# Kernel tuning notes

Measured on AMD Instinct MI355X. Metric: run time of the kernel, lower is better.

## Reference

```python
import jax, jax.numpy as jnp
import numpy as np

BATCH = 8
N_CLASSES = 3            # including background
PRE_NMS_LIMIT = 6000
NMS_THRESH = 0.5
SCALE = 512.0
WINDOW = (0.0, 0.0, 512.0, 512.0)   # y1, x1, y2, x2
STD_DEV = np.array([0.1, 0.1, 0.2, 0.2], np.float32)
GROUP_OFFSET = 4096.0    # > image extent; separates (batch, class) groups in NMS

_RATIOS = np.array([0.5, 1.0, 2.0])
_LEVELS = [((128, 128), 4, 8.0), ((64, 64), 8, 16.0), ((32, 32), 16, 32.0), ((16, 16), 32, 64.0)]


def _gen_anchors():
    # faithful port of generate_pyramid_anchors / generate_anchors (anchor_stride=1)
    out = []
    for (fy, fx), stride, scale in _LEVELS:
        s, r = np.meshgrid(np.array([scale]), _RATIOS)
        s, r = s.flatten(), r.flatten()
        heights = s / np.sqrt(r)
        widths = s * np.sqrt(r)
        sy = np.arange(fy) * stride
        sx = np.arange(fx) * stride
        sx, sy = np.meshgrid(sx, sy)
        bw, bcx = np.meshgrid(widths, sx)
        bh, bcy = np.meshgrid(heights, sy)
        centers = np.stack([bcy, bcx], axis=2).reshape(-1, 2)
        sizes = np.stack([bh, bw], axis=2).reshape(-1, 2)
        out.append(np.concatenate([centers - 0.5 * sizes, centers + 0.5 * sizes], axis=1))
    return np.concatenate(out, axis=0).astype(np.float32)  # (65280, 4) yxyx


def setup_inputs() -> dict:
    key = jax.random.key(0)
    k1, k2 = jax.random.split(key)
    anchors = jnp.asarray(_gen_anchors())
    n_anchors = anchors.shape[0]
    n_prop = BATCH * n_anchors
    logits = jax.random.normal(k1, (n_prop, N_CLASSES), jnp.float32)
    probs = jax.nn.softmax(logits, axis=-1)
    deltas = jax.random.normal(k2, (n_prop, 4), jnp.float32)
    batch_ixs = jnp.repeat(jnp.arange(BATCH, dtype=jnp.int64), n_anchors)
    return {"probs": probs, "deltas": deltas, "anchors": anchors, "batch_ixs": batch_ixs}


def _apply_box_deltas_2d(boxes, deltas):
    # boxes: (K,4) yxyx (normalized); deltas: (K,4) dy,dx,dh,dw
    h = boxes[:, 2] - boxes[:, 0]
    w = boxes[:, 3] - boxes[:, 1]
    cy = boxes[:, 0] + 0.5 * h + deltas[:, 0] * h
    cx = boxes[:, 1] + 0.5 * w + deltas[:, 1] * w
    h = h * jnp.exp(deltas[:, 2])
    w = w * jnp.exp(deltas[:, 3])
    y1 = cy - 0.5 * h
    x1 = cx - 0.5 * w
    return jnp.stack([y1, x1, y1 + h, x1 + w], axis=1)


def _nms_keep(boxes, thresh):
    # boxes (K,4), already sorted by score descending; returns bool keep mask.
    y1, x1, y2, x2 = boxes[:, 0], boxes[:, 1], boxes[:, 2], boxes[:, 3]
    areas = (y2 - y1 + 1.0) * (x2 - x1 + 1.0)
    ih = jnp.clip(jnp.minimum(y2[:, None], y2[None, :]) - jnp.maximum(y1[:, None], y1[None, :]) + 1.0, 0.0)
    iw = jnp.clip(jnp.minimum(x2[:, None], x2[None, :]) - jnp.maximum(x1[:, None], x1[None, :]) + 1.0, 0.0)
    inter = ih * iw
    iou = inter / (areas[:, None] + areas[None, :] - inter)  # (K,K)
    K = boxes.shape[0]
    idx = jnp.arange(K)

    def body(i, keep):
        sup = (iou[i] >= thresh) & (idx > i) & keep[i]
        return keep & ~sup

    return jax.lax.fori_loop(0, K, body, jnp.ones((K,), bool))


def reference(probs, deltas, anchors, batch_ixs):
    n_anchors = anchors.shape[0]
    n_fg = probs.shape[1] - 1
    # trim to top pre_nms_limit foreground scores (flat over proposals x fg classes)
    fg = probs[:, 1:].reshape(-1)
    scores, flat_ix = jax.lax.top_k(fg, PRE_NMS_LIMIT)  # sorted descending
    prop_ix = flat_ix // n_fg
    class_ids = flat_ix % n_fg + 1
    b = batch_ixs[prop_ix]
    a = anchors[prop_ix % n_anchors]        # anchors tiled per batch element
    d = deltas[prop_ix] * jnp.asarray(STD_DEV)
    rois = _apply_box_deltas_2d(a / SCALE, d) * SCALE
    lo = jnp.array([WINDOW[0], WINDOW[1], WINDOW[0], WINDOW[1]], rois.dtype)
    hi = jnp.array([WINDOW[2], WINDOW[3], WINDOW[2], WINDOW[3]], rois.dtype)
    rois = jnp.clip(rois, lo, hi)
    # batched per-class NMS: offset boxes so different (batch, class) groups never overlap
    group = (b * (n_fg + 1) + class_ids).astype(rois.dtype) * GROUP_OFFSET
    keep = _nms_keep(rois + group[:, None], NMS_THRESH)
    detections = jnp.concatenate(
        [rois, scores[:, None], keep.astype(rois.dtype)[:, None]], axis=1)  # (K, 6)
    return detections, class_ids, b
```

## Files before the change

kernel.cpp:

```cpp
#include <hip/hip_runtime.h>
#include <math.h>

typedef unsigned int u32;
typedef unsigned short u16;
typedef unsigned long long u64;

#define PRE_NMS 6000
#define NBLK    94
#define KMAX    640
#define MSTRIDE 11
#define MAXW    10
#define MTILE   (MAXW * MAXW)
#define FINEB   8192
#define LOWB    8064
#define TOTB    (FINEB + LOWB)
#define NHB     16
#define CANDMAX 16384
#define SLICES  8
#define NGRP    24
#define CBLK    256
#define CBUF    512
#define FLOOR_BITS 0x3F000000u

#define CTR_OFF    0
#define RANKS_OFF  256
#define PART_OFF   65792
#define CAND_OFF   1106176
#define BOXR_OFF   1237248
#define GBITS_OFF  1333504
#define KG_OFF     1351936
#define GRANKG_OFF 1352192
#define BOXG_OFF   1413632
#define AREAG_OFF  1659392
#define MASKG_OFF  1720832

__global__ __launch_bounds__(1024) void hist_kernel(const float4* __restrict__ probs4,
                                                    u32* __restrict__ partials, int n_prop) {
    __shared__ u32 hf[FINEB];
    __shared__ u32 hl[2][LOWB];
    int t = threadIdx.x;
    for (int i = t; i < FINEB; i += 1024) hf[i] = 0u;
    for (int i = t; i < 2 * LOWB; i += 1024) ((u32*)hl)[i] = 0u;
    __syncthreads();
    u32* l = hl[(t >> 6) & 1];
    int nq = n_prop >> 2;
    int idx = blockIdx.x * 1024 + t;
    int stride = gridDim.x * 1024;
    for (int q = idx; q < nq; q += stride) {
        float4 a = probs4[3 * q + 0];
        float4 b = probs4[3 * q + 1];
        float4 c = probs4[3 * q + 2];
        float vs[8] = {a.y, a.z, b.x, b.y, b.w, c.x, c.z, c.w};
        #pragma unroll
        for (int e = 0; e < 8; ++e) {
            u32 bits = __float_as_uint(vs[e]);
            if (bits >= FLOOR_BITS) {
                u32 fb = (bits - FLOOR_BITS) >> 10; if (fb >= FINEB) fb = FINEB - 1;
                atomicAdd(&hf[fb], 1u);
            } else {
                atomicAdd(&l[bits >> 17], 1u);
            }
        }
    }
    __syncthreads();
    u32* outp = partials + blockIdx.x * TOTB;
    for (int b = t; b < FINEB; b += 1024) outp[b] = hf[b];
    for (int b = t; b < LOWB; b += 1024) outp[FINEB + b] = hl[0][b] + hl[1][b];
}

__global__ __launch_bounds__(1024) void pivot_kernel(const u32* __restrict__ partials,
                                                     u32* __restrict__ ctr,
                                                     u32* __restrict__ ranks,
                                                     u32* __restrict__ gbits) {
    __shared__ u32 fh[FINEB];
    __shared__ u32 sd[1024];
    int t = threadIdx.x;
    for (int i = t; i < CANDMAX; i += 1024) ranks[i] = 0u;
    for (int i = t; i < NGRP * 192; i += 1024) gbits[i] = 0u;
    if (t == 0) ctr[0] = 0u;
    for (int b = t; b < FINEB; b += 1024) {
        u32 s = 0;
        #pragma unroll
        for (int k = 0; k < NHB; ++k) s += partials[k * TOTB + b];
        fh[b] = s;
    }
    __syncthreads();
    int hi = FINEB - 1 - 8 * t;
    u32 L = 0;
    #pragma unroll
    for (int e = 0; e < 8; ++e) L += fh[hi - e];
    sd[t] = L;
    __syncthreads();
    for (int off = 1; off < 1024; off <<= 1) {
        u32 x = (t >= off) ? sd[t - off] : 0u;
        __syncthreads();
        sd[t] += x;
        __syncthreads();
    }
    u32 incl = sd[t], excl = incl - L;
    u32 fineTotal = sd[1023];
    if (excl < (u32)PRE_NMS && incl >= (u32)PRE_NMS) {
        u32 run = excl;
        #pragma unroll
        for (int e = 0; e < 8; ++e) {
            u32 c = fh[hi - e];
            if (run < (u32)PRE_NMS && run + c >= (u32)PRE_NMS)
                ctr[1] = FLOOR_BITS + ((u32)(hi - e) << 10);
            run += c;
        }
    }
    if (fineTotal >= (u32)PRE_NMS) return;

    u32 rem = (u32)PRE_NMS - fineTotal;
    __syncthreads();
    for (int b = t; b < FINEB; b += 1024) {
        u32 s = 0;
        if (b < LOWB) {
            #pragma unroll
            for (int k = 0; k < NHB; ++k) s += partials[k * TOTB + FINEB + b];
        }
        fh[b] = s;
    }
    __syncthreads();
    L = 0;
    #pragma unroll
    for (int e = 0; e < 8; ++e) L += fh[hi - e];
    sd[t] = L;
    __syncthreads();
    for (int off = 1; off < 1024; off <<= 1) {
        u32 x = (t >= off) ? sd[t - off] : 0u;
        __syncthreads();
        sd[t] += x;
        __syncthreads();
    }
    incl = sd[t]; excl = incl - L;
    if (excl < rem && incl >= rem) {
        u32 run = excl;
        #pragma unroll
        for (int e = 0; e < 8; ++e) {
            u32 c = fh[hi - e];
            if (run < rem && run + c >= rem)
                ctr[1] = ((u32)(hi - e)) << 17;
            run += c;
        }
    }
}

__global__ __launch_bounds__(256) void compact_kernel(const float4* __restrict__ probs4,
                                                      u32* ctr, u64* __restrict__ cand,
                                                      int n_prop) {
    __shared__ u64 sloc[CBUF];
    __shared__ u32 scnt, sbase;
    int t = threadIdx.x;
    if (t == 0) scnt = 0u;
    __syncthreads();
    u32 pivot = ctr[1];
    int nq = n_prop >> 2;
    int idx = blockIdx.x * 256 + t;
    int stride = gridDim.x * 256;
    for (int q = idx; q < nq; q += stride) {
        float4 a = probs4[3 * q + 0];
        float4 b = probs4[3 * q + 1];
        float4 c = probs4[3 * q + 2];
        float vs[8] = {a.y, a.z, b.x, b.y, b.w, c.x, c.z, c.w};
        #pragma unroll
        for (int e = 0; e < 8; ++e) {
            u32 bits = __float_as_uint(vs[e]);
            if (bits >= pivot) {
                u32 lp = atomicAdd(&scnt, 1u);
                u32 i = (u32)(8 * q + e);
                if (lp < (u32)CBUF) sloc[lp] = ((u64)bits << 32) | (u64)(~i);
            }
        }
    }
    __syncthreads();
    u32 cnt = scnt; if (cnt > (u32)CBUF) cnt = (u32)CBUF;
    if (t == 0) sbase = atomicAdd(&ctr[0], cnt);
    __syncthreads();
    u32 base = sbase;
    for (u32 j = t; j < cnt; j += 256) {
        u32 pos = base + j;
        if (pos < (u32)CANDMAX) cand[pos] = sloc[j];
    }
}

__global__ __launch_bounds__(256) void rank_kernel(const u64* __restrict__ cand,
                                                   const u32* __restrict__ ctr,
                                                   u32* __restrict__ ranks) {
    __shared__ u64 tile[256];
    int t = threadIdx.x;
    u32 M = ctr[0]; if (M > (u32)CANDMAX) M = (u32)CANDMAX;
    int kb = blockIdx.y;
    if ((u32)(kb * 256) >= M) return;
    int i = kb * 256 + t;
    u64 key = (i < (int)M) ? cand[i] : 0ull;
    u32 Ls = (M + SLICES - 1) / SLICES;
    u32 s0 = blockIdx.x * Ls;
    u32 s1 = s0 + Ls; if (s1 > M) s1 = M;
    int cnt = 0;
    for (u32 base = s0; base < s1; base += 256) {
        u32 idx = base + t;
        tile[t] = (idx < s1) ? cand[idx] : 0ull;
        __syncthreads();
        #pragma unroll 8
        for (int q = 0; q < 256; ++q) cnt += (tile[q] > key) ? 1 : 0;
        __syncthreads();
    }
    if (i < (int)M && cnt > 0) atomicAdd(&ranks[i], (u32)cnt);
}

__global__ __launch_bounds__(256) void decode_kernel(const u64* __restrict__ cand,
                                                     const u32* __restrict__ ranks,
                                                     const u32* __restrict__ ctr,
                                                     const float4* __restrict__ deltas4,
                                                     const float4* __restrict__ anchors4,
                                                     float4* __restrict__ boxr,
                                                     u32* __restrict__ gbits,
                                                     float* __restrict__ out,
                                                     int n_anch) {
    u32 i = blockIdx.x * 256 + threadIdx.x;
    u32 M = ctr[0]; if (M > (u32)CANDMAX) M = (u32)CANDMAX;
    if (i >= M) return;
    u32 r = ranks[i];
    if (r >= (u32)PRE_NMS) return;
    u64 key = cand[i];
    u32 bits = (u32)(key >> 32);
    u32 flat = ~((u32)key);
    int p = (int)(flat >> 1);
    int cls = (int)(flat & 1u) + 1;
    int b = p / n_anch;
    int g = b * 3 + cls;
    int aidx = p - b * n_anch;
    float score = __uint_as_float(bits);
    float4 a = anchors4[aidx];
    float4 d = deltas4[p];
    float d0 = d.x * 0.1f, d1 = d.y * 0.1f, d2 = d.z * 0.2f, d3 = d.w * 0.2f;
    float y1 = a.x * (1.0f / 512.0f), x1 = a.y * (1.0f / 512.0f);
    float y2 = a.z * (1.0f / 512.0f), x2 = a.w * (1.0f / 512.0f);
    float h = y2 - y1, w = x2 - x1;
    float cy = y1 + 0.5f * h + d0 * h;
    float cx = x1 + 0.5f * w + d1 * w;
    h = h * expf(d2);
    w = w * expf(d3);
    float ry1 = (cy - 0.5f * h) * 512.0f;
    float rx1 = (cx - 0.5f * w) * 512.0f;
    float ry2 = (cy - 0.5f * h + h) * 512.0f;
    float rx2 = (cx - 0.5f * w + w) * 512.0f;
    ry1 = fminf(fmaxf(ry1, 0.0f), 512.0f);
    rx1 = fminf(fmaxf(rx1, 0.0f), 512.0f);
    ry2 = fminf(fmaxf(ry2, 0.0f), 512.0f);
    rx2 = fminf(fmaxf(rx2, 0.0f), 512.0f);
    out[r * 6 + 0] = ry1;
    out[r * 6 + 1] = rx1;
    out[r * 6 + 2] = ry2;
    out[r * 6 + 3] = rx2;
    out[r * 6 + 4] = score;
    out[r * 6 + 5] = 1.0f;
    out[PRE_NMS * 6 + r] = (float)cls;
    out[PRE_NMS * 7 + r] = (float)b;
    boxr[r] = make_float4(ry1, rx1, ry2, rx2);
    atomicOr(&gbits[g * 192 + (r >> 5)], 1u << (r & 31));
}

__global__ __launch_bounds__(512) void prep_kernel(const u32* __restrict__ gbits,
                                                   const float4* __restrict__ boxr,
                                                   u32* __restrict__ kg,
                                                   u32* __restrict__ grankg,
                                                   float4* __restrict__ boxg,
                                                   float* __restrict__ areag) {
    __shared__ int bpre[96];
    __shared__ u16 grankS[KMAX];
    __shared__ int sK;
    int g = blockIdx.x, t = threadIdx.x, lane = t & 63, wv = t >> 6;
    const u32* rb32 = gbits + g * 192;

    if (t < 64) {
        u64 w0 = (u64)rb32[2 * lane] | ((u64)rb32[2 * lane + 1] << 32);
        u64 w1 = (lane < NBLK - 64)
                 ? ((u64)rb32[128 + 2 * lane] | ((u64)rb32[129 + 2 * lane] << 32)) : 0ull;
        int c0 = (int)__popcll(w0), c1 = (int)__popcll(w1);
        int i0 = c0, i1 = c1;
        #pragma unroll
        for (int off = 1; off < 64; off <<= 1) {
            int a = __shfl_up(i0, off); if (lane >= off) i0 += a;
            int b = __shfl_up(i1, off); if (lane >= off) i1 += b;
        }
        int tot0 = __shfl(i0, 63), tot1 = __shfl(i1, 63);
        bpre[lane] = i0 - c0;
        if (lane < 32) bpre[64 + lane] = tot0 + ((lane < NBLK - 64) ? (i1 - c1) : 0);
        if (lane == 0) { sK = tot0 + tot1; kg[g] = (u32)(tot0 + tot1); }
    }
    __syncthreads();
    int K = sK;
    if (K == 0) return;
    int Kc = (K < KMAX) ? K : KMAX;

    for (int blk = wv; blk < NBLK; blk += 8) {
        u64 wmask = (u64)rb32[2 * blk] | ((u64)rb32[2 * blk + 1] << 32);
        if ((wmask >> lane) & 1ull) {
            int pos = bpre[blk] + (int)__popcll(wmask & ((1ull << lane) - 1ull));
            if (pos < KMAX) grankS[pos] = (u16)((blk << 6) | lane);
        }
    }
    __syncthreads();

    float4* bg = boxg + g * KMAX;
    float*  ag = areag + g * KMAX;
    u32*    gr = grankg + g * KMAX;
    for (int m = t; m < KMAX; m += 512) {
        if (m < Kc) {
            int r = grankS[m];
            float4 bb = boxr[r];
            bg[m] = bb;
            ag[m] = (bb.z - bb.x + 1.0f) * (bb.w - bb.y + 1.0f);
            gr[m] = (u32)r;
        } else {
            bg[m] = make_float4(-3e30f, -3e30f, -3e30f, -3e30f);
            ag[m] = 3e38f;
        }
    }
}

__global__ __launch_bounds__(64) void mask_kernel(const u32* __restrict__ kg,
                                                  const float4* __restrict__ boxg,
                                                  const float* __restrict__ areag,
                                                  u64* __restrict__ maskg) {
    int g = blockIdx.y;
    u32 K = kg[g];
    if (K == 0u) return;
    int Kc = (K < (u32)KMAX) ? (int)K : KMAX;
    int W = (Kc + 63) >> 6;
    int u = blockIdx.x;
    int c = u / MAXW, rbk = u % MAXW;
    if (c >= W || rbk >= W) return;
    int lane = threadIdx.x;
    int r = rbk * 64 + lane;
    u64* mg = maskg + (size_t)g * (KMAX * MSTRIDE);
    if (rbk > c) { mg[r * MSTRIDE + c] = 0ull; return; }
    int j0 = c << 6;
    const float4* bg = boxg + g * KMAX;
    const float*  ag = areag + g * KMAX;
    float4 rb = bg[r];
    float  ra = ag[r];
    float4 cb = bg[j0 + lane];
    float  ca = ag[j0 + lane];
    u64 word = 0ull;
    #pragma unroll 8
    for (int q = 0; q < 64; ++q) {
        float cbx = __shfl(cb.x, q);
        float cby = __shfl(cb.y, q);
        float cbz = __shfl(cb.z, q);
        float cbw = __shfl(cb.w, q);
        float cav = __shfl(ca, q);
        float ih = fminf(rb.z, cbz) - fmaxf(rb.x, cbx) + 1.0f;
        float iw = fminf(rb.w, cbw) - fmaxf(rb.y, cby) + 1.0f;
        ih = fmaxf(ih, 0.0f); iw = fmaxf(iw, 0.0f);
        bool o = (3.0f * ih * iw >= ra + cav) && ((j0 + q) > r);
        if (o) word |= (1ull << q);
    }
    mg[r * MSTRIDE + c] = word;
}

__global__ __launch_bounds__(512) void greedy_kernel(const u32* __restrict__ kg,
                                                     const u32* __restrict__ grankg,
                                                     const u64* __restrict__ maskg,
                                                     float* __restrict__ out) {
    __shared__ u64 maskm[KMAX * MSTRIDE + 64];
    __shared__ u16 grank[KMAX];
    int g = blockIdx.x, t = threadIdx.x, lane = t & 63;
    u32 K = kg[g];
    if (K == 0u) return;
    int Kc = (K < (u32)KMAX) ? (int)K : KMAX;
    int W = (Kc + 63) >> 6;
    const u64* mg = maskg + (size_t)g * (KMAX * MSTRIDE);
    int nw = Kc * MSTRIDE;
    for (int m = t; m < nw; m += 512) maskm[m] = mg[m];
    for (int m = nw + t; m < nw + 64; m += 512) maskm[m] = 0ull;
    for (int m = t; m < Kc; m += 512) grank[m] = (u16)grankg[g * KMAX + m];
    __syncthreads();

    if (t >= 64) return;
    u64 remv = 0ull;
    for (int w = 0; w < W; ++w) {
        int r0 = w << 6;
        int rend = Kc - r0; if (rend > 64) rend = 64;
        u64 curw = __shfl(remv, w);
        u64 kb = 0ull;
        for (int b0 = 0; b0 < rend; b0 += 8) {
            int n = rend - b0; if (n > 8) n = 8;
            u64 mrow[8], dg[8];
            #pragma unroll
            for (int j = 0; j < 8; ++j) {
                int rr = r0 + b0 + ((j < n) ? j : 0);
                mrow[j] = maskm[rr * MSTRIDE + lane];
                dg[j]   = maskm[rr * MSTRIDE + w];
            }
            #pragma unroll
            for (int j = 0; j < 8; ++j) {
                if (j < n) {
                    int b = b0 + j;
                    u64 km = ((curw >> b) & 1ull) ? 0ull : ~0ull;
                    curw |= dg[j] & km;
                    remv |= mrow[j] & km;
                    kb |= km & (1ull << b);
                }
            }
        }
        if (lane < rend)
            out[(int)grank[r0 + lane] * 6 + 5] = ((kb >> lane) & 1ull) ? 1.0f : 0.0f;
    }
}

extern "C" void kernel_launch(void* const* d_in, const int* in_sizes, int n_in,
                              void* d_out, int out_size, void* d_ws, size_t ws_size,
                              hipStream_t stream) {
    const float*  probs    = (const float*)d_in[0];
    const float4* deltas4  = (const float4*)d_in[1];
    const float4* anchors4 = (const float4*)d_in[2];
    int n_prop = in_sizes[1] / 4;
    int n_anch = in_sizes[2] / 4;

    char* ws = (char*)d_ws;
    u32* ctr      = (u32*)(ws + CTR_OFF);
    u32* ranks    = (u32*)(ws + RANKS_OFF);
    u32* partials = (u32*)(ws + PART_OFF);
    u64* cand     = (u64*)(ws + CAND_OFF);
    float4* boxr  = (float4*)(ws + BOXR_OFF);
    u32* gbits    = (u32*)(ws + GBITS_OFF);
    u32* kg       = (u32*)(ws + KG_OFF);
    u32* grankg   = (u32*)(ws + GRANKG_OFF);
    float4* boxg  = (float4*)(ws + BOXG_OFF);
    float* areag  = (float*)(ws + AREAG_OFF);
    u64* maskg    = (u64*)(ws + MASKG_OFF);
    float* out    = (float*)d_out;

    hist_kernel<<<NHB, 1024, 0, stream>>>((const float4*)probs, partials, n_prop);
    pivot_kernel<<<1, 1024, 0, stream>>>(partials, ctr, ranks, gbits);
    compact_kernel<<<CBLK, 256, 0, stream>>>((const float4*)probs, ctr, cand, n_prop);
    rank_kernel<<<dim3(SLICES, 64), 256, 0, stream>>>(cand, ctr, ranks);
    decode_kernel<<<CANDMAX / 256, 256, 0, stream>>>(cand, ranks, ctr, deltas4, anchors4,
                                                     boxr, gbits, out, n_anch);
    prep_kernel<<<NGRP, 512, 0, stream>>>(gbits, boxr, kg, grankg, boxg, areag);
    mask_kernel<<<dim3(MTILE, NGRP), 64, 0, stream>>>(kg, boxg, areag, maskg);
    greedy_kernel<<<NGRP, 512, 0, stream>>>(kg, grankg, maskg, out);
}
```

Baseline: 153.5 us.

## Replace all-pairs candidate ranking with bucket-scatter and in-bucket ranking

The pivot kernel now writes an exclusive prefix offset for every histogram bucket. Compaction scatters each candidate straight into its bucket's slot range using a global per-bucket atomic counter. Ranking then compares only against other members of the same bucket, replacing the O(M^2) all-pairs rank kernel, and rank is fused into decode. Prep and mask are merged into one kernel that keeps boxes in shared memory, and the histogram block count is doubled. Together these remove two launches and a quadratic compare, at the cost of global atomics in scatter and a serial scan for large buckets.

```diff
diff --git a/kernel.cpp b/kernel.cpp
--- a/kernel.cpp
+++ b/kernel.cpp
@@ -9,30 +9,32 @@
 #define NBLK    94
 #define KMAX    640
 #define MSTRIDE 11
-#define MAXW    10
-#define MTILE   (MAXW * MAXW)
 #define FINEB   8192
 #define LOWB    8064
 #define TOTB    (FINEB + LOWB)
-#define NHB     16
+#define NHB     32
 #define CANDMAX 16384
-#define SLICES  8
 #define NGRP    24
-#define CBLK    256
-#define CBUF    512
 #define FLOOR_BITS 0x3F000000u
 
 #define CTR_OFF    0
-#define RANKS_OFF  256
-#define PART_OFF   65792
-#define CAND_OFF   1106176
-#define BOXR_OFF   1237248
-#define GBITS_OFF  1333504
-#define KG_OFF     1351936
-#define GRANKG_OFF 1352192
-#define BOXG_OFF   1413632
-#define AREAG_OFF  1659392
-#define MASKG_OFF  1720832
+#define CAND_OFF   256
+#define BOXR_OFF   131328
+#define GBITS_OFF  227584
+#define KG_OFF     246016
+#define GRANKG_OFF 246272
+#define MASKG_OFF  307712
+#define BASE_OFF   1659392
+#define BCNT_OFF   1724928
+#define PART_OFF   1790464
+
+__device__ __forceinline__ u32 bucket_of(u32 bits) {
+    if (bits >= FLOOR_BITS) {
+        u32 fb = (bits - FLOOR_BITS) >> 10; if (fb > FINEB - 1) fb = FINEB - 1;
+        return fb;
+    }
+    return 8192u + (bits >> 17);
+}
 
 __global__ __launch_bounds__(1024) void hist_kernel(const float4* __restrict__ probs4,
                                                     u32* __restrict__ partials, int n_prop) {
@@ -70,14 +72,15 @@
 
 __global__ __launch_bounds__(1024) void pivot_kernel(const u32* __restrict__ partials,
                                                      u32* __restrict__ ctr,
-                                                     u32* __restrict__ ranks,
+                                                     u32* __restrict__ base,
+                                                     u32* __restrict__ bcnt,
                                                      u32* __restrict__ gbits) {
     __shared__ u32 fh[FINEB];
     __shared__ u32 sd[1024];
     int t = threadIdx.x;
-    for (int i = t; i < CANDMAX; i += 1024) ranks[i] = 0u;
+    for (int i = t; i < 16384; i += 1024) bcnt[i] = 0u;
     for (int i = t; i < NGRP * 192; i += 1024) gbits[i] = 0u;
-    if (t == 0) ctr[0] = 0u;
+    if (t == 0) { ctr[0] = 0u; ctr[1] = 0u; }
     for (int b = t; b < FINEB; b += 1024) {
         u32 s = 0;
         #pragma unroll
@@ -99,13 +102,18 @@
     }
     u32 incl = sd[t], excl = incl - L;
     u32 fineTotal = sd[1023];
-    if (excl < (u32)PRE_NMS && incl >= (u32)PRE_NMS) {
+    {
         u32 run = excl;
         #pragma unroll
         for (int e = 0; e < 8; ++e) {
-            u32 c = fh[hi - e];
-            if (run < (u32)PRE_NMS && run + c >= (u32)PRE_NMS)
-                ctr[1] = FLOOR_BITS + ((u32)(hi - e) << 10);
+            int fb = hi - e;
+            base[fb] = run;
+            u32 c = fh[fb];
+            if (run < (u32)PRE_NMS && run + c >= (u32)PRE_NMS) {
+                ctr[1] = FLOOR_BITS + ((u32)fb << 10);
+                u32 m = run + c; if (m > (u32)CANDMAX) m = (u32)CANDMAX;
+                ctr[0] = m;
+            }
             run += c;
         }
     }
@@ -134,29 +142,32 @@
         __syncthreads();
     }
     incl = sd[t]; excl = incl - L;
-    if (excl < rem && incl >= rem) {
+    {
         u32 run = excl;
         #pragma unroll
         for (int e = 0; e < 8; ++e) {
-            u32 c = fh[hi - e];
-            if (run < rem && run + c >= rem)
-                ctr[1] = ((u32)(hi - e)) << 17;
+            int lb = hi - e;
+            base[8192 + lb] = fineTotal + run;
+            u32 c = fh[lb];
+            if (run < rem && run + c >= rem) {
+                ctr[1] = ((u32)lb) << 17;
+                u32 m = fineTotal + run + c; if (m > (u32)CANDMAX) m = (u32)CANDMAX;
+                ctr[0] = m;
+            }
             run += c;
         }
     }
 }
 
-__global__ __launch_bounds__(256) void compact_kernel(const float4* __restrict__ probs4,
-                                                      u32* ctr, u64* __restrict__ cand,
+__global__ __launch_bounds__(256) void scatter_kernel(const float4* __restrict__ probs4,
+                                                      const u32* __restrict__ ctr,
+                                                      const u32* __restrict__ base,
+                                                      u32* __restrict__ bcnt,
+                                                      u64* __restrict__ cand,
                                                       int n_prop) {
-    __shared__ u64 sloc[CBUF];
-    __shared__ u32 scnt, sbase;
-    int t = threadIdx.x;
-    if (t == 0) scnt = 0u;
-    __syncthreads();
     u32 pivot = ctr[1];
     int nq = n_prop >> 2;
-    int idx = blockIdx.x * 256 + t;
+    int idx = blockIdx.x * 256 + threadIdx.x;
     int stride = gridDim.x * 256;
     for (int q = idx; q < nq; q += stride) {
         float4 a = probs4[3 * q + 0];
@@ -167,64 +178,42 @@
         for (int e = 0; e < 8; ++e) {
             u32 bits = __float_as_uint(vs[e]);
             if (bits >= pivot) {
-                u32 lp = atomicAdd(&scnt, 1u);
+                u32 bk = bucket_of(bits);
+                u32 off = atomicAdd(&bcnt[bk], 1u);
+                u32 slot = base[bk] + off;
                 u32 i = (u32)(8 * q + e);
-                if (lp < (u32)CBUF) sloc[lp] = ((u64)bits << 32) | (u64)(~i);
-            }
-        }
-    }
-    __syncthreads();
-    u32 cnt = scnt; if (cnt > (u32)CBUF) cnt = (u32)CBUF;
-    if (t == 0) sbase = atomicAdd(&ctr[0], cnt);
-    __syncthreads();
-    u32 base = sbase;
-    for (u32 j = t; j < cnt; j += 256) {
-        u32 pos = base + j;
-        if (pos < (u32)CANDMAX) cand[pos] = sloc[j];
-    }
-}
-
-__global__ __launch_bounds__(256) void rank_kernel(const u64* __restrict__ cand,
-                                                   const u32* __restrict__ ctr,
-                                                   u32* __restrict__ ranks) {
-    __shared__ u64 tile[256];
-    int t = threadIdx.x;
+                if (slot < (u32)CANDMAX) cand[slot] = ((u64)bits << 32) | (u64)(~i);
+            }
+        }
+    }
+}
+
+__global__ __launch_bounds__(256) void rankdecode_kernel(const u64* __restrict__ cand,
+                                                         const u32* __restrict__ ctr,
+                                                         const u32* __restrict__ base,
+                                                         const u32* __restrict__ bcnt,
+                                                         const float4* __restrict__ deltas4,
+                                                         const float4* __restrict__ anchors4,
+                                                         float4* __restrict__ boxr,
+                                                         u32* __restrict__ gbits,
+                                                         float* __restrict__ out,
+                                                         int n_anch) {
     u32 M = ctr[0]; if (M > (u32)CANDMAX) M = (u32)CANDMAX;
-    int kb = blockIdx.y;
-    if ((u32)(kb * 256) >= M) return;
-    int i = kb * 256 + t;
-    u64 key = (i < (int)M) ? cand[i] : 0ull;
-    u32 Ls = (M + SLICES - 1) / SLICES;
-    u32 s0 = blockIdx.x * Ls;
-    u32 s1 = s0 + Ls; if (s1 > M) s1 = M;
-    int cnt = 0;
-    for (u32 base = s0; base < s1; base += 256) {
-        u32 idx = base + t;
-        tile[t] = (idx < s1) ? cand[idx] : 0ull;
-        __syncthreads();
-        #pragma unroll 8
-        for (int q = 0; q < 256; ++q) cnt += (tile[q] > key) ? 1 : 0;
-        __syncthreads();
-    }
-    if (i < (int)M && cnt > 0) atomicAdd(&ranks[i], (u32)cnt);
-}
-
-__global__ __launch_bounds__(256) void decode_kernel(const u64* __restrict__ cand,
-                                                     const u32* __restrict__ ranks,
-                                                     const u32* __restrict__ ctr,
-                                                     const float4* __restrict__ deltas4,
-                                                     const float4* __restrict__ anchors4,
-                                                     float4* __restrict__ boxr,
-                                                     u32* __restrict__ gbits,
-                                                     float* __restrict__ out,
-                                                     int n_anch) {
     u32 i = blockIdx.x * 256 + threadIdx.x;
-    u32 M = ctr[0]; if (M > (u32)CANDMAX) M = (u32)CANDMAX;
     if (i >= M) return;
-    u32 r = ranks[i];
-    if (r >= (u32)PRE_NMS) return;
     u64 key = cand[i];
     u32 bits = (u32)(key >> 32);
+    u32 bk = bucket_of(bits);
+    u32 b0 = base[bk];
+    u32 n = bcnt[bk];
+    u32 r = b0;
+    if (n > 1) {
+        u32 end = b0 + n; if (end > M) end = M;
+        u32 cnt = 0;
+        for (u32 j = b0; j < end; ++j) cnt += (cand[j] > key) ? 1u : 0u;
+        r = b0 + cnt;
+    }
+    if (r >= (u32)PRE_NMS) return;
     u32 flat = ~((u32)key);
     int p = (int)(flat >> 1);
     int cls = (int)(flat & 1u) + 1;
@@ -262,14 +251,15 @@
     atomicOr(&gbits[g * 192 + (r >> 5)], 1u << (r & 31));
 }
 
-__global__ __launch_bounds__(512) void prep_kernel(const u32* __restrict__ gbits,
-                                                   const float4* __restrict__ boxr,
-                                                   u32* __restrict__ kg,
-                                                   u32* __restrict__ grankg,
-                                                   float4* __restrict__ boxg,
-                                                   float* __restrict__ areag) {
+__global__ __launch_bounds__(512) void prepmask_kernel(const u32* __restrict__ gbits,
+                                                       const float4* __restrict__ boxr,
+                                                       u32* __restrict__ kg,
+                                                       u32* __restrict__ grankg,
+                                                       u64* __restrict__ maskg) {
     __shared__ int bpre[96];
     __shared__ u16 grankS[KMAX];
+    __shared__ float4 sbox[KMAX];
+    __shared__ float sarea[KMAX];
     __shared__ int sK;
     int g = blockIdx.x, t = threadIdx.x, lane = t & 63, wv = t >> 6;
     const u32* rb32 = gbits + g * 192;
@@ -294,6 +284,7 @@
     int K = sK;
     if (K == 0) return;
     int Kc = (K < KMAX) ? K : KMAX;
+    int W = (Kc + 63) >> 6;
 
     for (int blk = wv; blk < NBLK; blk += 8) {
         u64 wmask = (u64)rb32[2 * blk] | ((u64)rb32[2 * blk + 1] << 32);
@@ -304,61 +295,46 @@
     }
     __syncthreads();
 
-    float4* bg = boxg + g * KMAX;
-    float*  ag = areag + g * KMAX;
-    u32*    gr = grankg + g * KMAX;
     for (int m = t; m < KMAX; m += 512) {
         if (m < Kc) {
             int r = grankS[m];
             float4 bb = boxr[r];
-            bg[m] = bb;
-            ag[m] = (bb.z - bb.x + 1.0f) * (bb.w - bb.y + 1.0f);
-            gr[m] = (u32)r;
+            sbox[m] = bb;
+            sarea[m] = (bb.z - bb.x + 1.0f) * (bb.w - bb.y + 1.0f);
+            grankg[g * KMAX + m] = (u32)r;
         } else {
-            bg[m] = make_float4(-3e30f, -3e30f, -3e30f, -3e30f);
-            ag[m] = 3e38f;
-        }
-    }
-}
-
-__global__ __launch_bounds__(64) void mask_kernel(const u32* __restrict__ kg,
-                                                  const float4* __restrict__ boxg,
-                                                  const float* __restrict__ areag,
-                                                  u64* __restrict__ maskg) {
-    int g = blockIdx.y;
-    u32 K = kg[g];
-    if (K == 0u) return;
-    int Kc = (K < (u32)KMAX) ? (int)K : KMAX;
-    int W = (Kc + 63) >> 6;
-    int u = blockIdx.x;
-    int c = u / MAXW, rbk = u % MAXW;
-    if (c >= W || rbk >= W) return;
-    int lane = threadIdx.x;
-    int r = rbk * 64 + lane;
+            sbox[m] = make_float4(-3e30f, -3e30f, -3e30f, -3e30f);
+            sarea[m] = 3e38f;
+        }
+    }
+    __syncthreads();
+
     u64* mg = maskg + (size_t)g * (KMAX * MSTRIDE);
-    if (rbk > c) { mg[r * MSTRIDE + c] = 0ull; return; }
-    int j0 = c << 6;
-    const float4* bg = boxg + g * KMAX;
-    const float*  ag = areag + g * KMAX;
-    float4 rb = bg[r];
-    float  ra = ag[r];
-    float4 cb = bg[j0 + lane];
-    float  ca = ag[j0 + lane];
-    u64 word = 0ull;
-    #pragma unroll 8
-    for (int q = 0; q < 64; ++q) {
-        float cbx = __shfl(cb.x, q);
-        float cby = __shfl(cb.y, q);
-        float cbz = __shfl(cb.z, q);
-        float cbw = __shfl(cb.w, q);
-        float cav = __shfl(ca, q);
-        float ih = fminf(rb.z, cbz) - fmaxf(rb.x, cbx) + 1.0f;
-        float iw = fminf(rb.w, cbw) - fmaxf(rb.y, cby) + 1.0f;
-        ih = fmaxf(ih, 0.0f); iw = fmaxf(iw, 0.0f);
-        bool o = (3.0f * ih * iw >= ra + cav) && ((j0 + q) > r);
-        if (o) word |= (1ull << q);
-    }
-    mg[r * MSTRIDE + c] = word;
+    for (int u = wv; u < W * W; u += 8) {
+        int c = u / W, rbk = u % W;
+        int r = rbk * 64 + lane;
+        if (rbk > c) { mg[r * MSTRIDE + c] = 0ull; continue; }
+        int j0 = c << 6;
+        float4 rb = sbox[r];
+        float  ra = sarea[r];
+        float4 cb = sbox[j0 + lane];
+        float  ca = sarea[j0 + lane];
+        u64 word = 0ull;
+        #pragma unroll 8
+        for (int q = 0; q < 64; ++q) {
+            float cbx = __shfl(cb.x, q);
+            float cby = __shfl(cb.y, q);
+            float cbz = __shfl(cb.z, q);
+            float cbw = __shfl(cb.w, q);
+            float cav = __shfl(ca, q);
+            float ih = fminf(rb.z, cbz) - fmaxf(rb.x, cbx) + 1.0f;
+            float iw = fminf(rb.w, cbw) - fmaxf(rb.y, cby) + 1.0f;
+            ih = fmaxf(ih, 0.0f); iw = fmaxf(iw, 0.0f);
+            bool o = (3.0f * ih * iw >= ra + cav) && ((j0 + q) > r);
+            if (o) word |= (1ull << q);
+        }
+        mg[r * MSTRIDE + c] = word;
+    }
 }
 
 __global__ __launch_bounds__(512) void greedy_kernel(const u32* __restrict__ kg,
@@ -422,25 +398,24 @@
 
     char* ws = (char*)d_ws;
     u32* ctr      = (u32*)(ws + CTR_OFF);
-    u32* ranks    = (u32*)(ws + RANKS_OFF);
-    u32* partials = (u32*)(ws + PART_OFF);
     u64* cand     = (u64*)(ws + CAND_OFF);
     float4* boxr  = (float4*)(ws + BOXR_OFF);
     u32* gbits    = (u32*)(ws + GBITS_OFF);
     u32* kg       = (u32*)(ws + KG_OFF);
     u32* grankg   = (u32*)(ws + GRANKG_OFF);
-    float4* boxg  = (float4*)(ws + BOXG_OFF);
-    float* areag  = (float*)(ws + AREAG_OFF);
     u64* maskg    = (u64*)(ws + MASKG_OFF);
+    u32* base     = (u32*)(ws + BASE_OFF);
+    u32* bcnt     = (u32*)(ws + BCNT_OFF);
+    u32* partials = (u32*)(ws + PART_OFF);
     float* out    = (float*)d_out;
 
     hist_kernel<<<NHB, 1024, 0, stream>>>((const float4*)probs, partials, n_prop);
-    pivot_kernel<<<1, 1024, 0, stream>>>(partials, ctr, ranks, gbits);
-    compact_kernel<<<CBLK, 256, 0, stream>>>((const float4*)probs, ctr, cand, n_prop);
-    rank_kernel<<<dim3(SLICES, 64), 256, 0, stream>>>(cand, ctr, ranks);
-    decode_kernel<<<CANDMAX / 256, 256, 0, stream>>>(cand, ranks, ctr, deltas4, anchors4,
-                                                     boxr, gbits, out, n_anch);
-    prep_kernel<<<NGRP, 512, 0, stream>>>(gbits, boxr, kg, grankg, boxg, areag);
-    mask_kernel<<<dim3(MTILE, NGRP), 64, 0, stream>>>(kg, boxg, areag, maskg);
+    pivot_kernel<<<1, 1024, 0, stream>>>(partials, ctr, base, bcnt, gbits);
+    scatter_kernel<<<128, 256, 0, stream>>>((const float4*)probs, ctr, base, bcnt,
+                                            cand, n_prop);
+    rankdecode_kernel<<<CANDMAX / 256, 256, 0, stream>>>(cand, ctr, base, bcnt,
+                                                         deltas4, anchors4,
+                                                         boxr, gbits, out, n_anch);
+    prepmask_kernel<<<NGRP, 512, 0, stream>>>(gbits, boxr, kg, grankg, maskg);
     greedy_kernel<<<NGRP, 512, 0, stream>>>(kg, grankg, maskg, out);
 }
```

Result: slower. 209.6 us (+36.6%).
